# Kernel optimization log

Measured on AMD Instinct MI355X. Metric: run time of the kernel, lower is better.

Reference implementation:

```python
import jax, jax.numpy as jnp
import numpy as np

T, B, F, H = 128, 32768, 8, 64


def gru_step(h, x, Wih, Whh, bih, bhh):
    # PyTorch GRU cell, gate order (r, z, n)
    gi = x @ Wih.T + bih          # [B, 3H]
    gh = h @ Whh.T + bhh          # [B, 3H]
    i_r, i_z, i_n = jnp.split(gi, 3, axis=-1)
    h_r, h_z, h_n = jnp.split(gh, 3, axis=-1)
    r = jax.nn.sigmoid(i_r + h_r)
    z = jax.nn.sigmoid(i_z + h_z)
    n = jnp.tanh(i_n + r * h_n)
    return (1.0 - z) * n + z * h


def setup_inputs() -> dict:
    key = jax.random.key(0)
    ks = jax.random.split(key, 12)
    s = 0.1  # small init scale
    return {
        "inputs": jax.random.normal(ks[0], (T, B, F), jnp.float32),
        "target": jax.random.normal(ks[1], (T, B, F), jnp.float32),
        "enc_Wih": jax.random.normal(ks[2], (3 * H, F), jnp.float32) * s,
        "enc_Whh": jax.random.normal(ks[3], (3 * H, H), jnp.float32) * s,
        "enc_bih": jax.random.normal(ks[4], (3 * H,), jnp.float32) * s,
        "enc_bhh": jax.random.normal(ks[5], (3 * H,), jnp.float32) * s,
        "dec_Wih": jax.random.normal(ks[6], (3 * H, F), jnp.float32) * s,
        "dec_Whh": jax.random.normal(ks[7], (3 * H, H), jnp.float32) * s,
        "dec_bih": jax.random.normal(ks[8], (3 * H,), jnp.float32) * s,
        "dec_bhh": jax.random.normal(ks[9], (3 * H,), jnp.float32) * s,
        "out_W": jax.random.normal(ks[10], (F, H), jnp.float32) * s,
        "out_b": jax.random.normal(ks[11], (F,), jnp.float32) * s,
    }


def reference(inputs, target, enc_Wih, enc_Whh, enc_bih, enc_bhh,
              dec_Wih, dec_Whh, dec_bih, dec_bhh, out_W, out_b):
    batch = inputs.shape[1]
    # ---- Encoder: single-layer GRU over T steps, h0 = 0 ----
    h0 = jnp.zeros((batch, H), inputs.dtype)

    def enc_body(h, x_t):
        h = gru_step(h, x_t, enc_Wih, enc_Whh, enc_bih, enc_bhh)
        return h, None

    enc_hidden, _ = jax.lax.scan(enc_body, h0, inputs)

    # ---- Decoder: teacher forcing; input at t=0 is zeros, then target[t-1] ----
    dec_in = jnp.concatenate(
        [jnp.zeros((1, batch, target.shape[2]), target.dtype), target[:-1]], axis=0)

    def dec_body(h, x_t):
        h = gru_step(h, x_t, dec_Wih, dec_Whh, dec_bih, dec_bhh)
        y = h @ out_W.T + out_b  # [B, F]
        return h, y

    _, decoder_outputs = jax.lax.scan(dec_body, enc_hidden, dec_in)
    return decoder_outputs  # [T, B, F]
```

## Files before the change

kernel.cpp:

```cpp
#include <hip/hip_runtime.h>

#define T_STEPS 128
#define B_SIZE  32768
#define F_DIM   8
#define H_DIM   64

#define BLOCK_THREADS 256
#define WAVES_PER_BLOCK 4
#define SAMPLES_PER_WAVE 16
#define GRID_BLOCKS (B_SIZE / (WAVES_PER_BLOCK * SAMPLES_PER_WAVE))

typedef float f32x4 __attribute__((ext_vector_type(4)));
typedef short bfrag __attribute__((ext_vector_type(8)));

#define MFMA16(A, B, C) __builtin_amdgcn_mfma_f32_16x16x32_bf16((A), (B), (C), 0, 0, 0)

__device__ __forceinline__ short f2bf(float f) {
    return __builtin_bit_cast(short, (__bf16)f);
}
__device__ __forceinline__ float sigf(float x) {
    return __builtin_amdgcn_rcpf(1.f + __expf(-x));
}
__device__ __forceinline__ float tanhf_fast(float x) {
    x = fminf(fmaxf(x, -15.f), 15.f);
    const float e = __expf(2.f * x);
    return 1.f - 2.f * __builtin_amdgcn_rcpf(e + 1.f);
}

struct Frags {
    bfrag wr[4][3];
    bfrag wz[4][3];
    bfrag whn[4][2];
    bfrag win[4];
    f32x4 bhn[4];
};

__device__ __forceinline__ void load_phase(Frags& F, const float* __restrict__ Wih,
                                           const float* __restrict__ Whh,
                                           const float* __restrict__ bih,
                                           const float* __restrict__ bhh,
                                           const int c, const int g) {
#pragma unroll
    for (int tt = 0; tt < 4; ++tt) {
        const int rowR = 16 * tt + c;
        const int rowZ = 64 + rowR;
        const int rowN = 128 + rowR;
#pragma unroll
        for (int kt = 0; kt < 2; ++kt) {
#pragma unroll
            for (int eh = 0; eh < 2; ++eh) {
#pragma unroll
                for (int ep = 0; ep < 2; ++ep) {
                    const int e = 4 * eh + 2 * ep;
                    const int k = 32 * kt + 16 * eh + 4 * g + 2 * ep;
                    const float2 vR = *(const float2*)(Whh + rowR * H_DIM + k);
                    const float2 vZ = *(const float2*)(Whh + rowZ * H_DIM + k);
                    const float2 vN = *(const float2*)(Whh + rowN * H_DIM + k);
                    F.wr[tt][kt][e]     = f2bf(vR.x);
                    F.wr[tt][kt][e + 1] = f2bf(vR.y);
                    F.wz[tt][kt][e]     = f2bf(vZ.x);
                    F.wz[tt][kt][e + 1] = f2bf(vZ.y);
                    F.whn[tt][kt][e]     = f2bf(vN.x);
                    F.whn[tt][kt][e + 1] = f2bf(vN.y);
                }
            }
        }
#pragma unroll
        for (int e = 0; e < 8; ++e) {
            const int k = 16 * (e >> 2) + 4 * g + (e & 3);
            float vR = 0.f, vZ = 0.f, vN = 0.f;
            if (k < 8) {
                vR = Wih[rowR * F_DIM + k];
                vZ = Wih[rowZ * F_DIM + k];
                vN = Wih[rowN * F_DIM + k];
            } else if (k == 8) {
                vR = bih[rowR] + bhh[rowR];
                vZ = bih[rowZ] + bhh[rowZ];
                vN = bih[rowN];
            }
            F.wr[tt][2][e] = f2bf(vR);
            F.wz[tt][2][e] = f2bf(vZ);
            F.win[tt][e]   = f2bf(vN);
        }
#pragma unroll
        for (int r = 0; r < 4; ++r)
            F.bhn[tt][r] = bhh[128 + 16 * tt + 4 * g + r];
    }
}

__device__ __forceinline__ void build_hB(bfrag (&hB)[2], const f32x4 (&hc)[4]) {
#pragma unroll
    for (int kt = 0; kt < 2; ++kt)
#pragma unroll
        for (int e = 0; e < 8; ++e)
            hB[kt][e] = f2bf(hc[2 * kt + (e >> 2)][e & 3]);
}

__device__ __forceinline__ void gru_step_m(const Frags& F, const bfrag (&hB)[2],
                                           const bfrag bx, f32x4 (&hc)[4]) {
#pragma unroll
    for (int tt = 0; tt < 4; ++tt) {
        f32x4 aR  = {0.f, 0.f, 0.f, 0.f};
        f32x4 aZ  = {0.f, 0.f, 0.f, 0.f};
        f32x4 aIN = {0.f, 0.f, 0.f, 0.f};
        f32x4 aHN = {0.f, 0.f, 0.f, 0.f};
        aR = MFMA16(F.wr[tt][0], hB[0], aR);
        aR = MFMA16(F.wr[tt][1], hB[1], aR);
        aR = MFMA16(F.wr[tt][2], bx,    aR);
        aZ = MFMA16(F.wz[tt][0], hB[0], aZ);
        aZ = MFMA16(F.wz[tt][1], hB[1], aZ);
        aZ = MFMA16(F.wz[tt][2], bx,    aZ);
        aHN = MFMA16(F.whn[tt][0], hB[0], aHN);
        aHN = MFMA16(F.whn[tt][1], hB[1], aHN);
        aIN = MFMA16(F.win[tt], bx, aIN);
#pragma unroll
        for (int r = 0; r < 4; ++r) {
            const float rg = sigf(aR[r]);
            const float zg = sigf(aZ[r]);
            const float ng = tanhf_fast(aIN[r] + rg * (aHN[r] + F.bhn[tt][r]));
            hc[tt][r] = ng + zg * (hc[tt][r] - ng);
        }
    }
}

__device__ __forceinline__ bfrag make_bx(const float4 xv) {
    bfrag bx;
#pragma unroll
    for (int e = 0; e < 4; ++e) bx[e] = f2bf(((const float*)&xv)[e]);
#pragma unroll
    for (int e = 4; e < 8; ++e) bx[e] = f2bf(0.f);
    return bx;
}

__global__ __launch_bounds__(BLOCK_THREADS, 2)
void seq2seq_mfma_kernel(const float* __restrict__ inputs, const float* __restrict__ target,
                         const float* __restrict__ eWih, const float* __restrict__ eWhh,
                         const float* __restrict__ ebih, const float* __restrict__ ebhh,
                         const float* __restrict__ dWih, const float* __restrict__ dWhh,
                         const float* __restrict__ dbih, const float* __restrict__ dbhh,
                         const float* __restrict__ oW, const float* __restrict__ ob,
                         float* __restrict__ out)
{
    const int tid  = threadIdx.x;
    const int lane = tid & 63;
    const int wv   = tid >> 6;
    const int c    = lane & 15;
    const int g    = lane >> 4;
    const long samp = ((long)blockIdx.x * WAVES_PER_BLOCK + wv) * SAMPLES_PER_WAVE + c;

    Frags F;
    load_phase(F, eWih, eWhh, ebih, ebhh, c, g);

    const float4 xconst = (g == 2) ? make_float4(1.f, 0.f, 0.f, 0.f)
                                   : make_float4(0.f, 0.f, 0.f, 0.f);

    f32x4 hc[4];
#pragma unroll
    for (int tt = 0; tt < 4; ++tt) hc[tt] = (f32x4){0.f, 0.f, 0.f, 0.f};
    bfrag hB[2];
    build_hB(hB, hc);

    float4 xn = xconst;
    if (g < 2) xn = *(const float4*)(inputs + samp * F_DIM + 4 * g);
#pragma unroll 1
    for (int t = 0; t < T_STEPS; ++t) {
        const float4 xv = xn;
        if (g < 2) {
            const int tn = (t + 1 < T_STEPS) ? t + 1 : t;
            xn = *(const float4*)(inputs + ((long)tn * B_SIZE + samp) * F_DIM + 4 * g);
        }
        const bfrag bx = make_bx(xv);
        gru_step_m(F, hB, bx, hc);
        build_hB(hB, hc);
    }

    load_phase(F, dWih, dWhh, dbih, dbhh, c, g);

    bfrag wout[2];
#pragma unroll
    for (int kt = 0; kt < 2; ++kt)
#pragma unroll
        for (int e = 0; e < 8; ++e) {
            const int k = 32 * kt + 16 * (e >> 2) + 4 * g + (e & 3);
            wout[kt][e] = f2bf((c < F_DIM) ? oW[c * H_DIM + k] : 0.f);
        }
    f32x4 obv;
#pragma unroll
    for (int r = 0; r < 4; ++r) obv[r] = (g < 2) ? ob[4 * g + r] : 0.f;

    xn = (g < 2) ? make_float4(0.f, 0.f, 0.f, 0.f) : xconst;
#pragma unroll 1
    for (int t = 0; t < T_STEPS; ++t) {
        const float4 xv = xn;
        if (g < 2 && t + 1 < T_STEPS) {
            xn = *(const float4*)(target + ((long)t * B_SIZE + samp) * F_DIM + 4 * g);
        }
        const bfrag bx = make_bx(xv);
        gru_step_m(F, hB, bx, hc);
        build_hB(hB, hc);

        f32x4 aO = {0.f, 0.f, 0.f, 0.f};
        aO = MFMA16(wout[0], hB[0], aO);
        aO = MFMA16(wout[1], hB[1], aO);
        if (g < 2) {
            float4 o;
            o.x = aO[0] + obv[0];
            o.y = aO[1] + obv[1];
            o.z = aO[2] + obv[2];
            o.w = aO[3] + obv[3];
            *(float4*)(out + ((long)t * B_SIZE + samp) * F_DIM + 4 * g) = o;
        }
    }
}

extern "C" void kernel_launch(void* const* d_in, const int* in_sizes, int n_in,
                              void* d_out, int out_size, void* d_ws, size_t ws_size,
                              hipStream_t stream) {
    (void)in_sizes; (void)n_in; (void)d_ws; (void)ws_size; (void)out_size;
    const float* inputs = (const float*)d_in[0];
    const float* target = (const float*)d_in[1];
    const float* eWih   = (const float*)d_in[2];
    const float* eWhh   = (const float*)d_in[3];
    const float* ebih   = (const float*)d_in[4];
    const float* ebhh   = (const float*)d_in[5];
    const float* dWih   = (const float*)d_in[6];
    const float* dWhh   = (const float*)d_in[7];
    const float* dbih   = (const float*)d_in[8];
    const float* dbhh   = (const float*)d_in[9];
    const float* oW     = (const float*)d_in[10];
    const float* ob     = (const float*)d_in[11];
    float* out = (float*)d_out;

    seq2seq_mfma_kernel<<<dim3(GRID_BLOCKS), dim3(BLOCK_THREADS), 0, stream>>>(
        inputs, target, eWih, eWhh, ebih, ebhh, dWih, dWhh, dbih, dbhh, oW, ob, out);
}
```

Before: 576.6 us.

## Split each 16-sample GRU across two waves with LDS hidden-state exchange

Each group of 16 samples is now handled by two waves, each owning half of the hidden units, and the two halves of the bf16 hidden state are swapped through double-buffered LDS with a block barrier every step. The input-projection fragments move to shared memory to cut register use, and launch bounds rise to 3 blocks per CU. Weights are prescaled by log2(e) so the activations can use exp2 directly, and the h_n bias is folded into the accumulator initialisation. This halves the serial MFMA and activation work per wave, paid for with a per-step __syncthreads, LDS traffic, and twice as many waves.

```diff
diff --git a/kernel.cpp b/kernel.cpp
--- a/kernel.cpp
+++ b/kernel.cpp
@@ -5,211 +5,180 @@
 #define F_DIM   8
 #define H_DIM   64
 
-#define BLOCK_THREADS 256
-#define WAVES_PER_BLOCK 4
-#define SAMPLES_PER_WAVE 16
-#define GRID_BLOCKS (B_SIZE / (WAVES_PER_BLOCK * SAMPLES_PER_WAVE))
+#define BLOCK_THREADS 128
+#define GRID_BLOCKS   (B_SIZE / 16)
 
 typedef float f32x4 __attribute__((ext_vector_type(4)));
 typedef short bfrag __attribute__((ext_vector_type(8)));
+typedef unsigned int u32x4 __attribute__((ext_vector_type(4)));
 
 #define MFMA16(A, B, C) __builtin_amdgcn_mfma_f32_16x16x32_bf16((A), (B), (C), 0, 0, 0)
 
-__device__ __forceinline__ short f2bf(float f) {
-    return __builtin_bit_cast(short, (__bf16)f);
-}
-__device__ __forceinline__ float sigf(float x) {
-    return __builtin_amdgcn_rcpf(1.f + __expf(-x));
-}
-__device__ __forceinline__ float tanhf_fast(float x) {
-    x = fminf(fmaxf(x, -15.f), 15.f);
-    const float e = __expf(2.f * x);
-    return 1.f - 2.f * __builtin_amdgcn_rcpf(e + 1.f);
-}
-
-struct Frags {
-    bfrag wr[4][3];
-    bfrag wz[4][3];
-    bfrag whn[4][2];
-    bfrag win[4];
-    f32x4 bhn[4];
-};
-
-__device__ __forceinline__ void load_phase(Frags& F, const float* __restrict__ Wih,
-                                           const float* __restrict__ Whh,
-                                           const float* __restrict__ bih,
-                                           const float* __restrict__ bhh,
-                                           const int c, const int g) {
-#pragma unroll
-    for (int tt = 0; tt < 4; ++tt) {
-        const int rowR = 16 * tt + c;
-        const int rowZ = 64 + rowR;
-        const int rowN = 128 + rowR;
-#pragma unroll
-        for (int kt = 0; kt < 2; ++kt) {
-#pragma unroll
-            for (int eh = 0; eh < 2; ++eh) {
-#pragma unroll
-                for (int ep = 0; ep < 2; ++ep) {
-                    const int e = 4 * eh + 2 * ep;
-                    const int k = 32 * kt + 16 * eh + 4 * g + 2 * ep;
-                    const float2 vR = *(const float2*)(Whh + rowR * H_DIM + k);
-                    const float2 vZ = *(const float2*)(Whh + rowZ * H_DIM + k);
-                    const float2 vN = *(const float2*)(Whh + rowN * H_DIM + k);
-                    F.wr[tt][kt][e]     = f2bf(vR.x);
-                    F.wr[tt][kt][e + 1] = f2bf(vR.y);
-                    F.wz[tt][kt][e]     = f2bf(vZ.x);
-                    F.wz[tt][kt][e + 1] = f2bf(vZ.y);
-                    F.whn[tt][kt][e]     = f2bf(vN.x);
-                    F.whn[tt][kt][e + 1] = f2bf(vN.y);
-                }
-            }
-        }
-#pragma unroll
-        for (int e = 0; e < 8; ++e) {
-            const int k = 16 * (e >> 2) + 4 * g + (e & 3);
-            float vR = 0.f, vZ = 0.f, vN = 0.f;
-            if (k < 8) {
-                vR = Wih[rowR * F_DIM + k];
-                vZ = Wih[rowZ * F_DIM + k];
-                vN = Wih[rowN * F_DIM + k];
-            } else if (k == 8) {
-                vR = bih[rowR] + bhh[rowR];
-                vZ = bih[rowZ] + bhh[rowZ];
-                vN = bih[rowN];
-            }
-            F.wr[tt][2][e] = f2bf(vR);
-            F.wz[tt][2][e] = f2bf(vZ);
-            F.win[tt][e]   = f2bf(vN);
-        }
-#pragma unroll
-        for (int r = 0; r < 4; ++r)
-            F.bhn[tt][r] = bhh[128 + 16 * tt + 4 * g + r];
-    }
-}
-
-__device__ __forceinline__ void build_hB(bfrag (&hB)[2], const f32x4 (&hc)[4]) {
-#pragma unroll
-    for (int kt = 0; kt < 2; ++kt)
-#pragma unroll
-        for (int e = 0; e < 8; ++e)
-            hB[kt][e] = f2bf(hc[2 * kt + (e >> 2)][e & 3]);
-}
-
-__device__ __forceinline__ void gru_step_m(const Frags& F, const bfrag (&hB)[2],
-                                           const bfrag bx, f32x4 (&hc)[4]) {
-#pragma unroll
-    for (int tt = 0; tt < 4; ++tt) {
-        f32x4 aR  = {0.f, 0.f, 0.f, 0.f};
-        f32x4 aZ  = {0.f, 0.f, 0.f, 0.f};
-        f32x4 aIN = {0.f, 0.f, 0.f, 0.f};
-        f32x4 aHN = {0.f, 0.f, 0.f, 0.f};
-        aR = MFMA16(F.wr[tt][0], hB[0], aR);
-        aR = MFMA16(F.wr[tt][1], hB[1], aR);
-        aR = MFMA16(F.wr[tt][2], bx,    aR);
-        aZ = MFMA16(F.wz[tt][0], hB[0], aZ);
-        aZ = MFMA16(F.wz[tt][1], hB[1], aZ);
-        aZ = MFMA16(F.wz[tt][2], bx,    aZ);
-        aHN = MFMA16(F.whn[tt][0], hB[0], aHN);
-        aHN = MFMA16(F.whn[tt][1], hB[1], aHN);
-        aIN = MFMA16(F.win[tt], bx, aIN);
-#pragma unroll
-        for (int r = 0; r < 4; ++r) {
-            const float rg = sigf(aR[r]);
-            const float zg = sigf(aZ[r]);
-            const float ng = tanhf_fast(aIN[r] + rg * (aHN[r] + F.bhn[tt][r]));
-            hc[tt][r] = ng + zg * (hc[tt][r] - ng);
-        }
-    }
-}
-
-__device__ __forceinline__ bfrag make_bx(const float4 xv) {
-    bfrag bx;
-#pragma unroll
-    for (int e = 0; e < 4; ++e) bx[e] = f2bf(((const float*)&xv)[e]);
-#pragma unroll
-    for (int e = 4; e < 8; ++e) bx[e] = f2bf(0.f);
-    return bx;
-}
-
-__global__ __launch_bounds__(BLOCK_THREADS, 2)
-void seq2seq_mfma_kernel(const float* __restrict__ inputs, const float* __restrict__ target,
-                         const float* __restrict__ eWih, const float* __restrict__ eWhh,
-                         const float* __restrict__ ebih, const float* __restrict__ ebhh,
-                         const float* __restrict__ dWih, const float* __restrict__ dWhh,
-                         const float* __restrict__ dbih, const float* __restrict__ dbhh,
-                         const float* __restrict__ oW, const float* __restrict__ ob,
-                         float* __restrict__ out)
+__device__ __forceinline__ short f2bf(float f) { return __builtin_bit_cast(short, (__bf16)f); }
+__device__ __forceinline__ float4 ld4(const void* p) { return *(const float4*)p; }
+
+constexpr float S1 = 1.4426950408889634f;
+constexpr float S2 = 2.f * S1;
+
+
+__global__ __launch_bounds__(BLOCK_THREADS, 3)
+void seq2seq_split_kernel(const float* __restrict__ inputs, const float* __restrict__ target,
+                          const float* __restrict__ eWih, const float* __restrict__ eWhh,
+                          const float* __restrict__ ebih, const float* __restrict__ ebhh,
+                          const float* __restrict__ dWih, const float* __restrict__ dWhh,
+                          const float* __restrict__ dbih, const float* __restrict__ dbhh,
+                          const float* __restrict__ oW, const float* __restrict__ ob,
+                          float* __restrict__ out)
 {
+    __shared__ u32x4 sXT[2][6][64];
+    __shared__ u32x4 sEx[2][2][64];
+
     const int tid  = threadIdx.x;
     const int lane = tid & 63;
-    const int wv   = tid >> 6;
+    const int w    = tid >> 6;
     const int c    = lane & 15;
     const int g    = lane >> 4;
-    const long samp = ((long)blockIdx.x * WAVES_PER_BLOCK + wv) * SAMPLES_PER_WAVE + c;
-
-    Frags F;
-    load_phase(F, eWih, eWhh, ebih, ebhh, c, g);
-
-    const float4 xconst = (g == 2) ? make_float4(1.f, 0.f, 0.f, 0.f)
-                                   : make_float4(0.f, 0.f, 0.f, 0.f);
-
-    f32x4 hc[4];
-#pragma unroll
-    for (int tt = 0; tt < 4; ++tt) hc[tt] = (f32x4){0.f, 0.f, 0.f, 0.f};
-    bfrag hB[2];
-    build_hB(hB, hc);
-
-    float4 xn = xconst;
-    if (g < 2) xn = *(const float4*)(inputs + samp * F_DIM + 4 * g);
+    const long samp = (long)blockIdx.x * 16 + c;
+
+    bfrag wr[2][2], wz[2][2], whn[2][2];
+    f32x4 bhn[2];
+
+    auto load_phase = [&](const float* __restrict__ Wih, const float* __restrict__ Whh,
+                          const float* __restrict__ bih, const float* __restrict__ bhh) {
+        __syncthreads();
+#pragma unroll
+        for (int tl = 0; tl < 2; ++tl) {
+            const int tt = 2 * w + tl;
+            const int rowR = 16 * tt + c, rowZ = rowR + 64, rowN = rowR + 128;
+#pragma unroll
+            for (int j = 0; j < 2; ++j) {
+                const int kt = (j == 0) ? w : 1 - w;
+                bfrag fr, fz, fn;
+#pragma unroll
+                for (int e = 0; e < 8; ++e) {
+                    const int k = 32 * kt + 16 * (e >> 2) + 4 * g + (e & 3);
+                    fr[e] = f2bf(Whh[rowR * H_DIM + k] * S1);
+                    fz[e] = f2bf(Whh[rowZ * H_DIM + k] * S1);
+                    fn[e] = f2bf(Whh[rowN * H_DIM + k] * S2);
+                }
+                wr[tl][j] = fr; wz[tl][j] = fz; whn[tl][j] = fn;
+            }
+            bfrag xr, xz, xnw;
+#pragma unroll
+            for (int e = 0; e < 8; ++e) {
+                const int k = 16 * (e >> 2) + 4 * g + (e & 3);
+                float vr = 0.f, vz = 0.f, vn = 0.f;
+                if (k < F_DIM) {
+                    vr = Wih[rowR * F_DIM + k]; vz = Wih[rowZ * F_DIM + k]; vn = Wih[rowN * F_DIM + k];
+                } else if (k == F_DIM) {
+                    vr = bih[rowR] + bhh[rowR]; vz = bih[rowZ] + bhh[rowZ]; vn = bih[rowN];
+                }
+                xr[e] = f2bf(vr * S1); xz[e] = f2bf(vz * S1); xnw[e] = f2bf(vn * S2);
+            }
+            sXT[w][3 * tl + 0][lane] = __builtin_bit_cast(u32x4, xr);
+            sXT[w][3 * tl + 1][lane] = __builtin_bit_cast(u32x4, xz);
+            sXT[w][3 * tl + 2][lane] = __builtin_bit_cast(u32x4, xnw);
+#pragma unroll
+            for (int r4 = 0; r4 < 4; ++r4) bhn[tl][r4] = bhh[128 + 16 * tt + 4 * g + r4] * S2;
+        }
+        __syncthreads();
+    };
+
+    f32x4 hc[2] = {{0.f, 0.f, 0.f, 0.f}, {0.f, 0.f, 0.f, 0.f}};
+    bfrag hl = (bfrag){0, 0, 0, 0, 0, 0, 0, 0};
+    bfrag ho = (bfrag){0, 0, 0, 0, 0, 0, 0, 0};
+    bfrag bx0 = (bfrag){0, 0, 0, 0, 0, 0, 0, 0};
+    if (g == 2) bx0[0] = f2bf(1.f);
+
+    const u32x4* xt = &sXT[w][0][lane];
+
+    auto step = [&](const bfrag bx) {
+#pragma unroll
+        for (int tl = 0; tl < 2; ++tl) {
+            const bfrag xr  = __builtin_bit_cast(bfrag, xt[(3 * tl + 0) * 64]);
+            const bfrag xz  = __builtin_bit_cast(bfrag, xt[(3 * tl + 1) * 64]);
+            const bfrag xnw = __builtin_bit_cast(bfrag, xt[(3 * tl + 2) * 64]);
+            f32x4 aR = {0.f, 0.f, 0.f, 0.f}, aZ = {0.f, 0.f, 0.f, 0.f};
+            f32x4 aIN = {0.f, 0.f, 0.f, 0.f};
+            f32x4 aHN = bhn[tl];
+            aR = MFMA16(wr[tl][0], hl, aR);  aR = MFMA16(wr[tl][1], ho, aR);  aR = MFMA16(xr, bx, aR);
+            aZ = MFMA16(wz[tl][0], hl, aZ);  aZ = MFMA16(wz[tl][1], ho, aZ);  aZ = MFMA16(xz, bx, aZ);
+            aHN = MFMA16(whn[tl][0], hl, aHN); aHN = MFMA16(whn[tl][1], ho, aHN);
+            aIN = MFMA16(xnw, bx, aIN);
+#pragma unroll
+            for (int r4 = 0; r4 < 4; ++r4) {
+                const float rg = __builtin_amdgcn_rcpf(1.f + __builtin_amdgcn_exp2f(-aR[r4]));
+                const float zg = __builtin_amdgcn_rcpf(1.f + __builtin_amdgcn_exp2f(-aZ[r4]));
+                const float np = aIN[r4] + rg * aHN[r4];
+                const float ng = 1.f - 2.f * __builtin_amdgcn_rcpf(__builtin_amdgcn_exp2f(np) + 1.f);
+                hc[tl][r4] = ng + zg * (hc[tl][r4] - ng);
+            }
+        }
+        bfrag nl;
+#pragma unroll
+        for (int e = 0; e < 8; ++e) nl[e] = f2bf(hc[e >> 2][e & 3]);
+        hl = nl;
+    };
+
+    load_phase(eWih, eWhh, ebih, ebhh);
+    int p = 0;
+    const unsigned istep = B_SIZE * F_DIM * 4;
+    unsigned ioff = (unsigned)((samp * F_DIM + 4 * g) * 4);
+    float4 xn = make_float4(0.f, 0.f, 0.f, 0.f);
+    if (g < 2) xn = ld4((const char*)inputs + ioff);
+    ioff += istep;
 #pragma unroll 1
     for (int t = 0; t < T_STEPS; ++t) {
         const float4 xv = xn;
-        if (g < 2) {
-            const int tn = (t + 1 < T_STEPS) ? t + 1 : t;
-            xn = *(const float4*)(inputs + ((long)tn * B_SIZE + samp) * F_DIM + 4 * g);
-        }
-        const bfrag bx = make_bx(xv);
-        gru_step_m(F, hB, bx, hc);
-        build_hB(hB, hc);
+        if (g < 2 && t + 1 < T_STEPS) xn = ld4((const char*)inputs + ioff);
+        ioff += istep;
+        bfrag bx = bx0;
+        if (g < 2) { bx[0] = f2bf(xv.x); bx[1] = f2bf(xv.y); bx[2] = f2bf(xv.z); bx[3] = f2bf(xv.w); }
+        step(bx);
+        sEx[p][w][lane] = __builtin_bit_cast(u32x4, hl);
+        __syncthreads();
+        ho = __builtin_bit_cast(bfrag, sEx[p][w ^ 1][lane]);
+        p ^= 1;
     }
 
-    load_phase(F, dWih, dWhh, dbih, dbhh, c, g);
-
-    bfrag wout[2];
-#pragma unroll
-    for (int kt = 0; kt < 2; ++kt)
+    load_phase(dWih, dWhh, dbih, dbhh);
+    bfrag wo[2];
+    f32x4 obv;
+#pragma unroll
+    for (int j = 0; j < 2; ++j)
 #pragma unroll
         for (int e = 0; e < 8; ++e) {
-            const int k = 32 * kt + 16 * (e >> 2) + 4 * g + (e & 3);
-            wout[kt][e] = f2bf((c < F_DIM) ? oW[c * H_DIM + k] : 0.f);
-        }
-    f32x4 obv;
-#pragma unroll
-    for (int r = 0; r < 4; ++r) obv[r] = (g < 2) ? ob[4 * g + r] : 0.f;
-
-    xn = (g < 2) ? make_float4(0.f, 0.f, 0.f, 0.f) : xconst;
+            const int k = 32 * j + 16 * (e >> 2) + 4 * g + (e & 3);
+            wo[j][e] = f2bf((c < F_DIM) ? oW[c * H_DIM + k] : 0.f);
+        }
+#pragma unroll
+    for (int r4 = 0; r4 < 4; ++r4) obv[r4] = (g < 2) ? ob[4 * g + r4] : 0.f;
+
+    unsigned toff = (unsigned)((samp * F_DIM + 4 * g) * 4);
+    unsigned ooff = toff;
+    xn = make_float4(0.f, 0.f, 0.f, 0.f);
 #pragma unroll 1
     for (int t = 0; t < T_STEPS; ++t) {
         const float4 xv = xn;
-        if (g < 2 && t + 1 < T_STEPS) {
-            xn = *(const float4*)(target + ((long)t * B_SIZE + samp) * F_DIM + 4 * g);
-        }
-        const bfrag bx = make_bx(xv);
-        gru_step_m(F, hB, bx, hc);
-        build_hB(hB, hc);
-
-        f32x4 aO = {0.f, 0.f, 0.f, 0.f};
-        aO = MFMA16(wout[0], hB[0], aO);
-        aO = MFMA16(wout[1], hB[1], aO);
-        if (g < 2) {
-            float4 o;
-            o.x = aO[0] + obv[0];
-            o.y = aO[1] + obv[1];
-            o.z = aO[2] + obv[2];
-            o.w = aO[3] + obv[3];
-            *(float4*)(out + ((long)t * B_SIZE + samp) * F_DIM + 4 * g) = o;
-        }
+        if (g < 2 && t + 1 < T_STEPS) xn = ld4((const char*)target + toff);
+        toff += istep;
+        bfrag bx = bx0;
+        if (g < 2) { bx[0] = f2bf(xv.x); bx[1] = f2bf(xv.y); bx[2] = f2bf(xv.z); bx[3] = f2bf(xv.w); }
+        step(bx);
+        sEx[p][w][lane] = __builtin_bit_cast(u32x4, hl);
+        __syncthreads();
+        ho = __builtin_bit_cast(bfrag, sEx[p][w ^ 1][lane]);
+        p ^= 1;
+        if (w == 0) {
+            f32x4 aO = obv;
+            aO = MFMA16(wo[0], hl, aO);
+            aO = MFMA16(wo[1], ho, aO);
+            if (g < 2) {
+                float4 o; o.x = aO[0]; o.y = aO[1]; o.z = aO[2]; o.w = aO[3];
+                *(float4*)((char*)out + ooff) = o;
+            }
+        }
+        ooff += istep;
     }
 }
 
@@ -231,6 +200,6 @@
     const float* ob     = (const float*)d_in[11];
     float* out = (float*)d_out;
 
-    seq2seq_mfma_kernel<<<dim3(GRID_BLOCKS), dim3(BLOCK_THREADS), 0, stream>>>(
+    seq2seq_split_kernel<<<dim3(GRID_BLOCKS), dim3(BLOCK_THREADS), 0, stream>>>(
         inputs, target, eWih, eWhh, ebih, ebhh, dWih, dWhh, dbih, dbhh, oW, ob, out);
 }
```

Result: faster. 479.3 us (-16.9%).
